# Performance work log

Hardware: AMD Instinct MI355X
Metric: run time of the kernel (lower is better)

The kernel has to match this reference:

```python
import jax, jax.numpy as jnp
import numpy as np

DIM = 192
HEADS = 8
B, H, W = 2, 256, 256
CPH = DIM // HEADS  # 24 channels per head
EPS = 1e-12

_SOB_DX = np.array([[1, 0, 1], [-2, 0, 2], [-1, 0, 1]], np.float32)
_SOB_DY = np.array([[1, -2, -1], [0, 0, 0], [1, 2, 1]], np.float32)


def _conv2d(x, w, pad, groups=1):
    return jax.lax.conv_general_dilated(
        x, w, window_strides=(1, 1), padding=[(pad, pad), (pad, pad)],
        dimension_numbers=('NCHW', 'OIHW', 'NCHW'), feature_group_count=groups)


def _l2norm(t):
    n = jnp.sqrt(jnp.sum(t * t, axis=-1, keepdims=True))
    return t / jnp.maximum(n, EPS)


def _topk_masked_softmax(attn, k):
    # attn: [B, HEADS, C, C]; keep top-k entries per row, softmax over them.
    b, h, c, _ = attn.shape
    idx = jax.lax.top_k(attn, k)[1]                      # [B,H,C,k]
    flat_idx = idx.reshape(-1, k)
    rows = jnp.arange(flat_idx.shape[0])[:, None]
    mask = jnp.zeros((b * h * c, c), bool).at[rows, flat_idx].set(True)
    masked = jnp.where(mask.reshape(attn.shape), attn, -jnp.inf)
    return jax.nn.softmax(masked, axis=-1)


def setup_inputs() -> dict:
    key = jax.random.key(0)
    ks = jax.random.split(key, 6)
    s = 0.02
    return {
        'x': jax.random.normal(ks[0], (B, DIM, H, W), jnp.float32),
        'q_w': jax.random.normal(ks[1], (DIM, DIM, 1, 1), jnp.float32) * s,
        'q_dw': jax.random.normal(ks[2], (DIM, 1, 3, 3), jnp.float32) * s,
        'kv_w': jax.random.normal(ks[3], (2 * DIM, DIM, 1, 1), jnp.float32) * s,
        'kv_dw': jax.random.normal(ks[4], (2 * DIM, 1, 3, 3), jnp.float32) * s,
        'proj_w': jax.random.normal(ks[5], (DIM, DIM, 1, 1), jnp.float32) * s,
        'temperature': jnp.ones((HEADS, 1, 1), jnp.float32),
        'a1': jnp.full((1,), 0.2, jnp.float32),
        'a2': jnp.full((1,), 0.2, jnp.float32),
        'a3': jnp.full((1,), 0.2, jnp.float32),
        'a4': jnp.full((1,), 0.2, jnp.float32),
    }


def reference(x, q_w, q_dw, kv_w, kv_dw, proj_w, temperature, a1, a2, a3, a4):
    b, c, h, w = x.shape
    # Sob: dense (dim,dim,3,3) Sobel convs (kernel broadcast over all in-channels)
    dx_w = jnp.broadcast_to(jnp.asarray(_SOB_DX), (c, c, 3, 3))
    dy_w = jnp.broadcast_to(jnp.asarray(_SOB_DY), (c, c, 3, 3))
    dx = _conv2d(x, dx_w, 1)
    dy = _conv2d(x, dy_w, 1)

    q_s = _conv2d(_conv2d(dx + dy, q_w, 0), q_dw, 1, groups=c)
    kv = _conv2d(_conv2d(x, kv_w, 0), kv_dw, 1, groups=2 * c)
    k_, v = kv[:, :c], kv[:, c:]

    hw = h * w
    q_s = _l2norm(q_s.reshape(b, HEADS, CPH, hw))
    k_ = _l2norm(k_.reshape(b, HEADS, CPH, hw))
    v = v.reshape(b, HEADS, CPH, hw)

    # channel attention: [B, HEADS, C, C]
    attn = jnp.einsum('bhcn,bhdn->bhcd', q_s, k_) * temperature

    C = CPH
    out = (a1 * (_topk_masked_softmax(attn, int(C / 2)) @ v)
           + a2 * (_topk_masked_softmax(attn, int(C * 2 / 3)) @ v)
           + a3 * (_topk_masked_softmax(attn, int(C * 3 / 4)) @ v)
           + a4 * (_topk_masked_softmax(attn, int(C * 4 / 5)) @ v))

    out = out.reshape(b, c, h, w)
    return _conv2d(out, proj_w, 0)
```

## Files before the change

### kernel.cpp

```cpp
#include <hip/hip_runtime.h>
#include <math.h>

#define NH 8
#define HWv 65536
#define C2 384

typedef __attribute__((ext_vector_type(8))) short bf16x8;
typedef __attribute__((ext_vector_type(4))) float f32x4;

__device__ __forceinline__ float bf2f(unsigned short u) {
    union { unsigned int i; float f; } v; v.i = ((unsigned int)u) << 16; return v.f;
}
__device__ __forceinline__ unsigned short f2bf(float f) {
    union { float f; unsigned int i; } v; v.f = f;
    unsigned int r = v.i + 0x7fff + ((v.i >> 16) & 1);
    return (unsigned short)(r >> 16);
}
__device__ __forceinline__ float hi_of(float a) {
    union { float f; unsigned int i; } u; u.f = a; u.i &= 0xffff0000u; return u.f;
}
__device__ __forceinline__ unsigned short hi16(float a) {
    union { float f; unsigned int i; } u; u.f = a; return (unsigned short)(u.i >> 16);
}
__device__ __forceinline__ unsigned int pack_hi2(float a, float b) {
    union { float f; unsigned int i; } ua, ub; ua.f = a; ub.f = b;
    return (ua.i >> 16) | (ub.i & 0xffff0000u);
}
__device__ __forceinline__ void gld16(const void* g, void* l) {
    __builtin_amdgcn_global_load_lds(
        (const __attribute__((address_space(1))) unsigned int*)g,
        (__attribute__((address_space(3))) unsigned int*)l, 16, 0, 0);
}
__device__ __forceinline__ int rot4(int lb, int row) {
    return (lb + row + (row >> 2)) & 3;
}

__global__ __launch_bounds__(256) void k_wprep(const float* __restrict__ w,
                                               const float* __restrict__ qw,
                                               unsigned short* __restrict__ oh,
                                               unsigned short* __restrict__ ol,
                                               float* __restrict__ qs) {
    if (blockIdx.x == 288) {
        const int o = threadIdx.x;
        if (o < 192) {
            float s = 0.f;
            for (int i = 0; i < 192; ++i) s += qw[(size_t)o * 192 + i];
            qs[o] = s;
        }
        return;
    }
    const int i = blockIdx.x * 256 + threadIdx.x;
    const int e = i & 7, jp = (i >> 3) & 3, rowidx = i >> 5;
    const int o = rowidx % 384, ks = rowidx / 384;
    const int lb = (jp - o - (o >> 2)) & 3;
    const int k = ks * 32 + (lb << 3) + e;
    const float v = w[(size_t)o * 192 + k];
    const unsigned short h = f2bf(v);
    oh[i] = h;
    ol[i] = f2bf(v - bf2f(h));
}

__global__ __launch_bounds__(256, 3) void k_gemm(const float* __restrict__ x,
                                                 const unsigned short* __restrict__ wh,
                                                 const unsigned short* __restrict__ wl,
                                                 unsigned short* __restrict__ t,
                                                 float* __restrict__ s) {
    const int l = blockIdx.x;
    const int xcd = l & 7, idx = l >> 3;
    const int pxtile = xcd * 64 + (idx >> 1);
    const int half = idx & 1;
    const int b = blockIdx.z;
    const int p0 = pxtile * 128;
    const int woff = half * 192;
    const int tid = threadIdx.x;
    const int lane = tid & 63, wv = tid >> 6;
    __shared__ __align__(16) char SU[40960];
    unsigned short* Xh  = (unsigned short*)SU;
    unsigned short* Xl  = Xh + 128 * 32;
    unsigned short* Whs = Xl + 128 * 32;
    unsigned short* Wls = Whs + 192 * 32;
    unsigned short* Ts  = (unsigned short*)SU;
    float* Ls = (float*)(SU + 26624);
    f32x4 acc[2][12];
#pragma unroll
    for (int m = 0; m < 2; ++m)
#pragma unroll
        for (int n = 0; n < 12; ++n) acc[m][n] = (f32x4){0.f, 0.f, 0.f, 0.f};
    const int px = tid & 127, cg = tid >> 7;
    const float* xb = x + (size_t)b * 192 * HWv + p0 + px;
    const int r = lane & 15, g = lane >> 4;
    const int pbx0 = rot4(2 * cg, px);
    const int pbx1 = rot4(2 * cg + 1, px);
    float csum = 0.f;
    for (int ks = 0; ks < 6; ++ks) {
        const int k0 = ks * 32;
        __syncthreads();
        {
            const char* gh  = (const char*)wh + ((size_t)(ks * 384 + woff)) * 64;
            const char* gl2 = (const char*)wl + ((size_t)(ks * 384 + woff)) * 64;
            char* lh = (char*)Whs;
            char* ll = (char*)Wls;
#pragma unroll
            for (int i = 0; i < 3; ++i) {
                const int chunk = (i * 4 + wv) * 1024;
                gld16(gh + chunk + lane * 16, lh + chunk);
                gld16(gl2 + chunk + lane * 16, ll + chunk);
            }
        }
        {
            unsigned int ph[8], pl[8];
#pragma unroll
            for (int i2 = 0; i2 < 8; ++i2) {
                const int c0 = k0 + cg * 16 + i2 * 2;
                const float v0 = xb[(size_t)c0 * HWv];
                const float v1 = xb[(size_t)(c0 + 1) * HWv];
                csum += v0 + v1;
                ph[i2] = pack_hi2(v0, v1);
                pl[i2] = pack_hi2(v0 - hi_of(v0), v1 - hi_of(v1));
            }
            *(uint4*)&Xh[px * 32 + pbx0 * 8] = make_uint4(ph[0], ph[1], ph[2], ph[3]);
            *(uint4*)&Xh[px * 32 + pbx1 * 8] = make_uint4(ph[4], ph[5], ph[6], ph[7]);
            *(uint4*)&Xl[px * 32 + pbx0 * 8] = make_uint4(pl[0], pl[1], pl[2], pl[3]);
            *(uint4*)&Xl[px * 32 + pbx1 * 8] = make_uint4(pl[4], pl[5], pl[6], pl[7]);
        }
        __syncthreads();
        bf16x8 ah[2], al[2];
#pragma unroll
        for (int m = 0; m < 2; ++m) {
            const int row = wv * 32 + m * 16 + r;
            const int ro = rot4(g, row) * 8;
            ah[m] = *(const bf16x8*)&Xh[row * 32 + ro];
            al[m] = *(const bf16x8*)&Xl[row * 32 + ro];
        }
#pragma unroll
        for (int n = 0; n < 12; ++n) {
            const int row = n * 16 + r;
            const int ro = rot4(g, row) * 8;
            const bf16x8 bh = *(const bf16x8*)&Whs[row * 32 + ro];
            const bf16x8 bl = *(const bf16x8*)&Wls[row * 32 + ro];
#pragma unroll
            for (int m = 0; m < 2; ++m) {
                acc[m][n] = __builtin_amdgcn_mfma_f32_16x16x32_bf16(ah[m], bh, acc[m][n], 0, 0, 0);
                acc[m][n] = __builtin_amdgcn_mfma_f32_16x16x32_bf16(ah[m], bl, acc[m][n], 0, 0, 0);
                acc[m][n] = __builtin_amdgcn_mfma_f32_16x16x32_bf16(al[m], bh, acc[m][n], 0, 0, 0);
            }
        }
    }
    __syncthreads();
    if (half == 0) Ls[cg * 128 + px] = csum;
    __syncthreads();
    if (half == 0 && tid < 128)
        s[((size_t)b << 16) + p0 + tid] = Ls[tid] + Ls[128 + tid];
    unsigned short* tb = t + (size_t)b * HWv * C2;
#pragma unroll
    for (int ph2 = 0; ph2 < 2; ++ph2) {
        __syncthreads();
        if ((wv >> 1) == ph2) {
            const int baser = (wv & 1) * 32;
#pragma unroll
            for (int m = 0; m < 2; ++m)
#pragma unroll
                for (int n = 0; n < 12; ++n)
#pragma unroll
                    for (int rr = 0; rr < 4; ++rr)
                        Ts[(baser + m * 16 + g * 4 + rr) * 200 + n * 16 + r] =
                            f2bf(acc[m][n][rr]);
        }
        __syncthreads();
        for (int i = tid; i < 1536; i += 256) {
            const int pxl = i / 24, cho = (i % 24) * 8;
            unsigned short* dst = tb + (size_t)(p0 + ph2 * 64 + pxl) * C2 + woff + cho;
            *(uint4*)dst = *(const uint4*)&Ts[pxl * 200 + cho];
        }
    }
}

__global__ __launch_bounds__(256) void k_attn(const unsigned short* __restrict__ t,
                                              const float* __restrict__ sbuf,
                                              const float* __restrict__ qsum,
                                              const float* __restrict__ qdw,
                                              const float* __restrict__ kvdw,
                                              float* __restrict__ part) {
    const int z = blockIdx.z, b = z >> 3, h = z & 7;
    const int tid = threadIdx.x;
    const int lane = tid & 63, wv = tid >> 6;
    __shared__ __align__(16) char U[50688];
    float* ehalo = (float*)U;
    float* Thalo = (float*)(U + 1296);
    float* shalo = (float*)(U + 32496);
    unsigned short* QKh = (unsigned short*)U;
    unsigned short* QKl = QKh + 48 * 264;
    float* Pp = (float*)U;
    __shared__ float qdwl[216], kdwl[216], qsml[24];
    for (int i = tid; i < 456; i += 256) {
        if (i < 216) qdwl[i] = qdw[h * 216 + i];
        else if (i < 432) kdwl[i - 216] = kvdw[h * 216 + (i - 216)];
        else qsml[i - 432] = qsum[h * 24 + (i - 432)];
    }
    f32x4 acc[6];
#pragma unroll
    for (int tl = 0; tl < 6; ++tl) acc[tl] = (f32x4){0.f, 0.f, 0.f, 0.f};
    const int lr = tid >> 4, lc = tid & 15;
    const int r = lane & 15, g = lane >> 4;
    for (int st = 0; st < 4; ++st) {
        const int tx0 = (blockIdx.x * 2 + (st & 1)) * 16;
        const int ty0 = (blockIdx.y * 2 + (st >> 1)) * 16;
        __syncthreads();
        for (int i = tid; i < 400; i += 256) {
            const int rr = i / 20, cc = i % 20;
            const int y = ty0 - 2 + rr, xx = tx0 - 2 + cc;
            shalo[i] = (y >= 0 && y < 256 && xx >= 0 && xx < 256)
                           ? sbuf[((size_t)b << 16) + y * 256 + xx] : 0.f;
        }
        for (int i = tid; i < 972; i += 256) {
            const int p = i / 3, seg = i % 3;
            const int rr = p / 18, cc = p % 18;
            const int y = ty0 - 1 + rr, xx = tx0 - 1 + cc;
            if (y >= 0 && y < 256 && xx >= 0 && xx < 256) {
                const unsigned short* src =
                    t + ((size_t)b * HWv + y * 256 + xx) * C2 + h * 24 + seg * 8;
                const uint4 v = *(const uint4*)src;
                Thalo[(seg * 8 + 0) * 325 + p] = bf2f((unsigned short)(v.x & 0xffff));
                Thalo[(seg * 8 + 1) * 325 + p] = bf2f((unsigned short)(v.x >> 16));
                Thalo[(seg * 8 + 2) * 325 + p] = bf2f((unsigned short)(v.y & 0xffff));
                Thalo[(seg * 8 + 3) * 325 + p] = bf2f((unsigned short)(v.y >> 16));
                Thalo[(seg * 8 + 4) * 325 + p] = bf2f((unsigned short)(v.z & 0xffff));
                Thalo[(seg * 8 + 5) * 325 + p] = bf2f((unsigned short)(v.z >> 16));
                Thalo[(seg * 8 + 6) * 325 + p] = bf2f((unsigned short)(v.w & 0xffff));
                Thalo[(seg * 8 + 7) * 325 + p] = bf2f((unsigned short)(v.w >> 16));
            } else {
#pragma unroll
                for (int j = 0; j < 8; ++j) Thalo[(seg * 8 + j) * 325 + p] = 0.f;
            }
        }
        __syncthreads();
        for (int i = tid; i < 324; i += 256) {
            const int rr = i / 18, cc = i % 18;
            const int y = ty0 - 1 + rr, xx = tx0 - 1 + cc;
            const float v = (((((shalo[rr * 20 + cc]
                              - shalo[rr * 20 + cc + 1])
                              - shalo[(rr + 1) * 20 + cc])
                              + shalo[(rr + 1) * 20 + cc + 2])
                              + shalo[(rr + 2) * 20 + cc + 1])
                              + shalo[(rr + 2) * 20 + cc + 2]);
            ehalo[i] = (y >= 0 && y < 256 && xx >= 0 && xx < 256) ? 2.f * v : 0.f;
        }
        __syncthreads();
        float qreg[24], kreg[24];
#pragma unroll
        for (int c = 0; c < 24; ++c) {
            float aq = 0.f, ak = 0.f;
#pragma unroll
            for (int dy = 0; dy < 3; ++dy)
#pragma unroll
                for (int dx = 0; dx < 3; ++dx) {
                    aq = fmaf(qdwl[c * 9 + dy * 3 + dx], ehalo[(lr + dy) * 18 + lc + dx], aq);
                    ak = fmaf(kdwl[c * 9 + dy * 3 + dx], Thalo[c * 325 + (lr + dy) * 18 + lc + dx], ak);
                }
            qreg[c] = qsml[c] * aq;
            kreg[c] = ak;
        }
        __syncthreads();
#pragma unroll
        for (int c = 0; c < 24; ++c) {
            const float q = qreg[c], kv = kreg[c];
            QKh[c * 264 + tid] = hi16(q);
            QKl[c * 264 + tid] = hi16(q - hi_of(q));
            QKh[(24 + c) * 264 + tid] = hi16(kv);
            QKl[(24 + c) * 264 + tid] = hi16(kv - hi_of(kv));
        }
        __syncthreads();
#pragma unroll
        for (int c2 = 0; c2 < 2; ++c2) {
            const int colb = (wv * 2 + c2) * 32 + g * 8;
            bf16x8 fh[3], fl[3];
#pragma unroll
            for (int rt = 0; rt < 3; ++rt) {
                fh[rt] = *(const bf16x8*)&QKh[(rt * 16 + r) * 264 + colb];
                fl[rt] = *(const bf16x8*)&QKl[(rt * 16 + r) * 264 + colb];
            }
#define GRAM(T, A, B) \
    acc[T] = __builtin_amdgcn_mfma_f32_16x16x32_bf16(fh[A], fh[B], acc[T], 0, 0, 0); \
    acc[T] = __builtin_amdgcn_mfma_f32_16x16x32_bf16(fh[A], fl[B], acc[T], 0, 0, 0); \
    acc[T] = __builtin_amdgcn_mfma_f32_16x16x32_bf16(fl[A], fh[B], acc[T], 0, 0, 0);
            GRAM(0, 0, 0) GRAM(1, 0, 1) GRAM(2, 0, 2)
            GRAM(3, 1, 1) GRAM(4, 1, 2) GRAM(5, 2, 2)
#undef GRAM
        }
    }
    __syncthreads();
#pragma unroll
    for (int tl = 0; tl < 6; ++tl)
#pragma unroll
        for (int reg = 0; reg < 4; ++reg)
            Pp[wv * 1536 + tl * 256 + (g * 4 + reg) * 16 + r] = acc[tl][reg];
    __syncthreads();
    float* dst = part + ((size_t)z * 64 + blockIdx.y * 8 + blockIdx.x) * 1536;
    for (int i = tid; i < 1536; i += 256)
        dst[i] = Pp[i] + Pp[1536 + i] + Pp[3072 + i] + Pp[4608 + i];
}

__device__ __forceinline__ int gidx(int i, int j) {
    const int rt = i >> 4, ct = j >> 4;
    const int tl = (rt == 0) ? ct : (rt == 1 ? 2 + ct : 5);
    return tl * 256 + (i & 15) * 16 + (j & 15);
}

__global__ __launch_bounds__(256) void k_redcomb(const float* __restrict__ part,
                                                 const float* __restrict__ temp,
                                                 const float* __restrict__ a1,
                                                 const float* __restrict__ a2,
                                                 const float* __restrict__ a3,
                                                 const float* __restrict__ a4,
                                                 float* __restrict__ Wg) {
    const int z = blockIdx.x, b = z >> 3, h = z & 7;
    const int tid = threadIdx.x;
    __shared__ float S[1536];
    __shared__ float att[24][24];
    __shared__ float nq[24], nk[24];
    for (int i = tid; i < 1536; i += 256) {
        float sum = 0.f;
        const float* p = part + (size_t)z * 64 * 1536 + i;
        for (int blk = 0; blk < 64; ++blk) sum += p[(size_t)blk * 1536];
        S[i] = sum;
    }
    __syncthreads();
    if (tid < 24) nq[tid] = fmaxf(sqrtf(S[gidx(tid, tid)]), 1e-12f);
    else if (tid >= 32 && tid < 56) {
        const int d = tid - 32;
        nk[d] = fmaxf(sqrtf(S[gidx(24 + d, 24 + d)]), 1e-12f);
    }
    __syncthreads();
    const float tp = temp[h];
    for (int op = tid; op < 576; op += 256) {
        const int c = op / 24, d = op % 24;
        att[c][d] = S[gidx(c, 24 + d)] * tp / (nq[c] * nk[d]);
    }
    __syncthreads();
    if (tid < 24) {
        const int c = tid;
        float v[24];
#pragma unroll
        for (int d = 0; d < 24; ++d) v[d] = att[c][d];
        int rank[24];
#pragma unroll
        for (int d = 0; d < 24; ++d) {
            int rr = 0;
#pragma unroll
            for (int d2 = 0; d2 < 24; ++d2)
                rr += (v[d2] > v[d]) || (v[d2] == v[d] && d2 < d);
            rank[d] = rr;
        }
        const int ks[4] = {12, 16, 18, 19};
        const float as[4] = {a1[0], a2[0], a3[0], a4[0]};
        float w[24] = {};
        for (int ti = 0; ti < 4; ++ti) {
            const int kk = ks[ti];
            float m = -1e30f;
            for (int d = 0; d < 24; ++d) if (rank[d] < kk) m = fmaxf(m, v[d]);
            float Z = 0.f, ex[24];
            for (int d = 0; d < 24; ++d) {
                ex[d] = (rank[d] < kk) ? expf(v[d] - m) : 0.f;
                Z += ex[d];
            }
            const float sc = as[ti] / Z;
            for (int d = 0; d < 24; ++d) w[d] += ex[d] * sc;
        }
        for (int d = 0; d < 24; ++d)
            Wg[(((size_t)b * NH + h) * 24 + c) * 24 + d] = w[d];
    }
}

__global__ void k_makeM(const float* __restrict__ projw, const float* __restrict__ Wg,
                        unsigned short* __restrict__ Mh, unsigned short* __restrict__ Ml) {
    const int b = blockIdx.x / 192, o = blockIdx.x % 192;
    const int j = threadIdx.x;
    const int h = j / 24, d = j % 24;
    float s = 0.f;
#pragma unroll
    for (int cc = 0; cc < 24; ++cc)
        s = fmaf(projw[(size_t)o * 192 + h * 24 + cc],
                 Wg[(((size_t)b * NH + h) * 24 + cc) * 24 + d], s);
    const unsigned short hh = f2bf(s);
    const int jg = j >> 5, jb = (j >> 3) & 3, e = j & 7;
    const int jp = rot4(jb, o);
    const size_t dst = (((size_t)b * 6 + jg) * 192 + o) * 32 + jp * 8 + e;
    Mh[dst] = hh;
    Ml[dst] = f2bf(s - bf2f(hh));
}

__global__ __launch_bounds__(256) void k_final(const unsigned short* __restrict__ t,
                                               const float* __restrict__ kvdw,
                                               const unsigned short* __restrict__ Mh,
                                               const unsigned short* __restrict__ Ml,
                                               float* __restrict__ out) {
    const int b = blockIdx.y;
    const int tile = blockIdx.x;
    const int x0 = (tile & 15) * 16, y0 = (tile >> 4) * 4;
    const int tid = threadIdx.x;
    const int lane = tid & 63, wv = tid >> 6;
    __shared__ __align__(16) unsigned short Th[108][40];
    __shared__ __align__(16) unsigned short Msh[192 * 32], Msl[192 * 32];
    __shared__ __align__(16) unsigned short Vsh[64][40], Vsl[64][40];
    __shared__ float Wdl[288];
    f32x4 acc[3][4];
#pragma unroll
    for (int m = 0; m < 3; ++m)
#pragma unroll
        for (int n = 0; n < 4; ++n) acc[m][n] = (f32x4){0.f, 0.f, 0.f, 0.f};
    const int px = tid & 63, jq = tid >> 6;
    const int lx = px & 15, ly = px >> 4;
    const int r = lane & 15, g = lane >> 4;
    for (int jg = 0; jg < 6; ++jg) {
        const int j0 = jg * 32;
        __syncthreads();
        {
            const char* gh  = (const char*)Mh + (((size_t)b * 6 + jg) * 192) * 64;
            const char* gl2 = (const char*)Ml + (((size_t)b * 6 + jg) * 192) * 64;
            char* lh = (char*)Msh;
            char* ll = (char*)Msl;
#pragma unroll
            for (int i = 0; i < 3; ++i) {
                const int chunk = (i * 4 + wv) * 1024;
                gld16(gh + chunk + lane * 16, lh + chunk);
                gld16(gl2 + chunk + lane * 16, ll + chunk);
            }
        }
        if (tid < 216) {
            const int hp = tid >> 1, half = tid & 1;
            const int hy = hp / 18, hx = hp % 18;
            const int y = y0 - 1 + hy, xx = x0 - 1 + hx;
            uint4 v0 = make_uint4(0, 0, 0, 0), v1 = make_uint4(0, 0, 0, 0);
            if (y >= 0 && y < 256 && xx >= 0 && xx < 256) {
                const unsigned short* src =
                    t + ((size_t)b * HWv + y * 256 + xx) * C2 + 192 + j0 + half * 16;
                v0 = *(const uint4*)src;
                v1 = *(const uint4*)(src + 8);
            }
            *(uint4*)&Th[hp][half * 16] = v0;
            *(uint4*)&Th[hp][half * 16 + 8] = v1;
        }
        for (int i = tid; i < 288; i += 256) Wdl[i] = kvdw[1728 + jg * 288 + i];
        __syncthreads();
        {
            float vv[8] = {0.f, 0.f, 0.f, 0.f, 0.f, 0.f, 0.f, 0.f};
#pragma unroll
            for (int dy = 0; dy < 3; ++dy)
#pragma unroll
                for (int dx = 0; dx < 3; ++dx) {
                    const int hp = (ly + dy) * 18 + lx + dx;
                    const uint4 tv = *(const uint4*)&Th[hp][jq * 8];
                    float tf[8];
                    tf[0] = bf2f((unsigned short)(tv.x & 0xffff));
                    tf[1] = bf2f((unsigned short)(tv.x >> 16));
                    tf[2] = bf2f((unsigned short)(tv.y & 0xffff));
                    tf[3] = bf2f((unsigned short)(tv.y >> 16));
                    tf[4] = bf2f((unsigned short)(tv.z & 0xffff));
                    tf[5] = bf2f((unsigned short)(tv.z >> 16));
                    tf[6] = bf2f((unsigned short)(tv.w & 0xffff));
                    tf[7] = bf2f((unsigned short)(tv.w >> 16));
                    const int tap = dy * 3 + dx;
#pragma unroll
                    for (int jj = 0; jj < 8; ++jj)
                        vv[jj] = fmaf(Wdl[(jq * 8 + jj) * 9 + tap], tf[jj], vv[jj]);
                }
            unsigned int ph[4], pl[4];
#pragma unroll
            for (int i2 = 0; i2 < 4; ++i2) {
                const float a = vv[i2 * 2], c = vv[i2 * 2 + 1];
                ph[i2] = pack_hi2(a, c);
                pl[i2] = pack_hi2(a - hi_of(a), c - hi_of(c));
            }
            *(uint4*)&Vsh[px][jq * 8] = make_uint4(ph[0], ph[1], ph[2], ph[3]);
            *(uint4*)&Vsl[px][jq * 8] = make_uint4(pl[0], pl[1], pl[2], pl[3]);
        }
        __syncthreads();
        bf16x8 bh[4], bl[4];
#pragma unroll
        for (int n = 0; n < 4; ++n) {
            bh[n] = *(const bf16x8*)&Vsh[n * 16 + r][g * 8];
            bl[n] = *(const bf16x8*)&Vsl[n * 16 + r][g * 8];
        }
#pragma unroll
        for (int m = 0; m < 3; ++m) {
            const int row = wv * 48 + m * 16 + r;
            const int ro = rot4(g, row) * 8;
            const bf16x8 ah = *(const bf16x8*)&Msh[row * 32 + ro];
            const bf16x8 al = *(const bf16x8*)&Msl[row * 32 + ro];
#pragma unroll
            for (int n = 0; n < 4; ++n) {
                acc[m][n] = __builtin_amdgcn_mfma_f32_16x16x32_bf16(ah, bh[n], acc[m][n], 0, 0, 0);
                acc[m][n] = __builtin_amdgcn_mfma_f32_16x16x32_bf16(ah, bl[n], acc[m][n], 0, 0, 0);
                acc[m][n] = __builtin_amdgcn_mfma_f32_16x16x32_bf16(al, bh[n], acc[m][n], 0, 0, 0);
            }
        }
    }
#pragma unroll
    for (int m = 0; m < 3; ++m) {
        const int o = wv * 48 + m * 16 + g * 4;
#pragma unroll
        for (int n = 0; n < 4; ++n) {
            const int p = (y0 + n) * 256 + x0 + r;
#pragma unroll
            for (int rr = 0; rr < 4; ++rr)
                out[((size_t)b * 192 + o + rr) * HWv + p] = acc[m][n][rr];
        }
    }
}


extern "C" void kernel_launch(void* const* d_in, const int* in_sizes, int n_in,
                              void* d_out, int out_size, void* d_ws, size_t ws_size,
                              hipStream_t stream) {
    (void)in_sizes; (void)n_in; (void)out_size;
    const float* x     = (const float*)d_in[0];
    const float* qw    = (const float*)d_in[1];
    const float* qdw   = (const float*)d_in[2];
    const float* kvw   = (const float*)d_in[3];
    const float* kvdw  = (const float*)d_in[4];
    const float* projw = (const float*)d_in[5];
    const float* temp  = (const float*)d_in[6];
    const float* a1    = (const float*)d_in[7];
    const float* a2    = (const float*)d_in[8];
    const float* a3    = (const float*)d_in[9];
    const float* a4    = (const float*)d_in[10];
    float* out = (float*)d_out;

    const size_t T_EL = (size_t)2 * HWv * C2;
    const size_t needB = T_EL * 2
                       + (size_t)(131072 + 131072 + 192 + 1572864 + 24576 + 9216) * 4
                       + (size_t)(73728 * 4) * 2;
    if (ws_size < needB) return;
    unsigned short* t = (unsigned short*)d_ws;
    float* s    = (float*)(t + T_EL);
    float* e    = s + 131072;
    float* qsum = e + 131072;
    float* part = qsum + 192;
    float* accS = part + 1572864;
    float* Wg   = accS + 24576;
    unsigned short* wh = (unsigned short*)(Wg + 9216);
    unsigned short* wl = wh + 73728;
    unsigned short* Mh = wl + 73728;
    unsigned short* Ml = Mh + 73728;

    k_wprep<<<289, 256, 0, stream>>>(kvw, qw, wh, wl, qsum);
    k_gemm<<<dim3(1024, 1, 2), 256, 0, stream>>>(x, wh, wl, t, s);
    k_attn<<<dim3(8, 8, 16), 256, 0, stream>>>(t, s, qsum, qdw, kvdw, part);
    k_redcomb<<<16, 256, 0, stream>>>(part, temp, a1, a2, a3, a4, Wg);
    k_makeM<<<384, 192, 0, stream>>>(projw, Wg, Mh, Ml);
    k_final<<<dim3(1024, 2), 256, 0, stream>>>(t, kvdw, Mh, Ml, out);
}
```

Baseline: 256.0 us.

## Double-buffer GEMM K-loop to overlap global loads with MFMA compute

The k_gemm main loop now uses two LDS buffers. It prefetches the next K-slice of x into registers and issues async weight loads into the alternate buffer, then runs the MFMAs on the current one, and packs x into the next buffer afterwards. This drops one barrier per iteration and hides global-load latency behind compute. In exchange, LDS per block doubles to 80 KB and launch bounds drop from 3 to 2 blocks per SM, which lowers occupancy and raises register pressure from the extra 16 prefetch registers.

```diff
diff --git a/kernel.cpp b/kernel.cpp
--- a/kernel.cpp
+++ b/kernel.cpp
@@ -60,7 +60,7 @@
     ol[i] = f2bf(v - bf2f(h));
 }
 
-__global__ __launch_bounds__(256, 3) void k_gemm(const float* __restrict__ x,
+__global__ __launch_bounds__(256, 2) void k_gemm(const float* __restrict__ x,
                                                  const unsigned short* __restrict__ wh,
                                                  const unsigned short* __restrict__ wl,
                                                  unsigned short* __restrict__ t,
@@ -74,12 +74,8 @@
     const int woff = half * 192;
     const int tid = threadIdx.x;
     const int lane = tid & 63, wv = tid >> 6;
-    __shared__ __align__(16) char SU[40960];
-    unsigned short* Xh  = (unsigned short*)SU;
-    unsigned short* Xl  = Xh + 128 * 32;
-    unsigned short* Whs = Xl + 128 * 32;
-    unsigned short* Wls = Whs + 192 * 32;
-    unsigned short* Ts  = (unsigned short*)SU;
+    __shared__ __align__(16) char SU[81920];
+    unsigned short* Ts = (unsigned short*)SU;
     float* Ls = (float*)(SU + 26624);
     f32x4 acc[2][12];
 #pragma unroll
@@ -92,38 +88,62 @@
     const int pbx0 = rot4(2 * cg, px);
     const int pbx1 = rot4(2 * cg + 1, px);
     float csum = 0.f;
+    float xr[16];
+
+    auto load_x = [&](int ks) {
+#pragma unroll
+        for (int i2 = 0; i2 < 8; ++i2) {
+            const int c0 = ks * 32 + cg * 16 + i2 * 2;
+            xr[2 * i2]     = xb[(size_t)c0 * HWv];
+            xr[2 * i2 + 1] = xb[(size_t)(c0 + 1) * HWv];
+        }
+    };
+    auto stage_w = [&](int ks, char* base) {
+        const char* gh  = (const char*)wh + ((size_t)(ks * 384 + woff)) * 64;
+        const char* gl2 = (const char*)wl + ((size_t)(ks * 384 + woff)) * 64;
+        char* lh = base + 16384;
+        char* ll = base + 28672;
+#pragma unroll
+        for (int i = 0; i < 3; ++i) {
+            const int chunk = (i * 4 + wv) * 1024;
+            gld16(gh + chunk + lane * 16, lh + chunk);
+            gld16(gl2 + chunk + lane * 16, ll + chunk);
+        }
+    };
+    auto pack_x = [&](char* base) {
+        unsigned short* Xh = (unsigned short*)base;
+        unsigned short* Xl = (unsigned short*)(base + 8192);
+        unsigned int ph[8], pl[8];
+#pragma unroll
+        for (int i2 = 0; i2 < 8; ++i2) {
+            const float v0 = xr[2 * i2], v1 = xr[2 * i2 + 1];
+            csum += v0 + v1;
+            ph[i2] = pack_hi2(v0, v1);
+            pl[i2] = pack_hi2(v0 - hi_of(v0), v1 - hi_of(v1));
+        }
+        *(uint4*)&Xh[px * 32 + pbx0 * 8] = make_uint4(ph[0], ph[1], ph[2], ph[3]);
+        *(uint4*)&Xh[px * 32 + pbx1 * 8] = make_uint4(ph[4], ph[5], ph[6], ph[7]);
+        *(uint4*)&Xl[px * 32 + pbx0 * 8] = make_uint4(pl[0], pl[1], pl[2], pl[3]);
+        *(uint4*)&Xl[px * 32 + pbx1 * 8] = make_uint4(pl[4], pl[5], pl[6], pl[7]);
+    };
+
+    load_x(0);
+    stage_w(0, SU);
+    pack_x(SU);
+    __syncthreads();
+
+#pragma unroll
     for (int ks = 0; ks < 6; ++ks) {
-        const int k0 = ks * 32;
-        __syncthreads();
-        {
-            const char* gh  = (const char*)wh + ((size_t)(ks * 384 + woff)) * 64;
-            const char* gl2 = (const char*)wl + ((size_t)(ks * 384 + woff)) * 64;
-            char* lh = (char*)Whs;
-            char* ll = (char*)Wls;
-#pragma unroll
-            for (int i = 0; i < 3; ++i) {
-                const int chunk = (i * 4 + wv) * 1024;
-                gld16(gh + chunk + lane * 16, lh + chunk);
-                gld16(gl2 + chunk + lane * 16, ll + chunk);
-            }
-        }
-        {
-            unsigned int ph[8], pl[8];
-#pragma unroll
-            for (int i2 = 0; i2 < 8; ++i2) {
-                const int c0 = k0 + cg * 16 + i2 * 2;
-                const float v0 = xb[(size_t)c0 * HWv];
-                const float v1 = xb[(size_t)(c0 + 1) * HWv];
-                csum += v0 + v1;
-                ph[i2] = pack_hi2(v0, v1);
-                pl[i2] = pack_hi2(v0 - hi_of(v0), v1 - hi_of(v1));
-            }
-            *(uint4*)&Xh[px * 32 + pbx0 * 8] = make_uint4(ph[0], ph[1], ph[2], ph[3]);
-            *(uint4*)&Xh[px * 32 + pbx1 * 8] = make_uint4(ph[4], ph[5], ph[6], ph[7]);
-            *(uint4*)&Xl[px * 32 + pbx0 * 8] = make_uint4(pl[0], pl[1], pl[2], pl[3]);
-            *(uint4*)&Xl[px * 32 + pbx1 * 8] = make_uint4(pl[4], pl[5], pl[6], pl[7]);
-        }
-        __syncthreads();
+        char* bc = SU + (ks & 1) * 40960;
+        char* bn = SU + ((ks & 1) ^ 1) * 40960;
+        if (ks < 5) {
+            load_x(ks + 1);
+            stage_w(ks + 1, bn);
+        }
+        unsigned short* Xh  = (unsigned short*)bc;
+        unsigned short* Xl  = (unsigned short*)(bc + 8192);
+        unsigned short* Whs = (unsigned short*)(bc + 16384);
+        unsigned short* Wls = (unsigned short*)(bc + 28672);
         bf16x8 ah[2], al[2];
 #pragma unroll
         for (int m = 0; m < 2; ++m) {
@@ -145,8 +165,10 @@
                 acc[m][n] = __builtin_amdgcn_mfma_f32_16x16x32_bf16(al[m], bh, acc[m][n], 0, 0, 0);
             }
         }
-    }
-    __syncthreads();
+        if (ks < 5) pack_x(bn);
+        __syncthreads();
+    }
+
     if (half == 0) Ls[cg * 128 + px] = csum;
     __syncthreads();
     if (half == 0 && tid < 128)
```

Result: slower. 263.7 us (+3.0%).

## Split k_gemm tile across 8 waves in a 4x2 wave grid

Applied to the files above, without the earlier changes.

Doubles the k_gemm block from 256 to 512 threads. Each wave now computes a 32x96 output sub-tile instead of 32x192, which halves the accumulator registers per wave and raises the wave count available for latency hiding. The global-to-LDS staging of the X slices and weight chunks is redistributed over the eight waves, and the per-pixel channel sums are reduced across four channel groups. The trade-off is that each wave reloads its A fragments for fewer MFMAs, and block-wide barriers now span more waves.

```diff
diff --git a/kernel.cpp b/kernel.cpp
--- a/kernel.cpp
+++ b/kernel.cpp
@@ -60,7 +60,7 @@
     ol[i] = f2bf(v - bf2f(h));
 }
 
-__global__ __launch_bounds__(256, 3) void k_gemm(const float* __restrict__ x,
+__global__ __launch_bounds__(512, 4) void k_gemm(const float* __restrict__ x,
                                                  const unsigned short* __restrict__ wh,
                                                  const unsigned short* __restrict__ wl,
                                                  unsigned short* __restrict__ t,
@@ -74,6 +74,7 @@
     const int woff = half * 192;
     const int tid = threadIdx.x;
     const int lane = tid & 63, wv = tid >> 6;
+    const int wm = wv & 3, wn = wv >> 2;
     __shared__ __align__(16) char SU[40960];
     unsigned short* Xh  = (unsigned short*)SU;
     unsigned short* Xl  = Xh + 128 * 32;
@@ -81,16 +82,15 @@
     unsigned short* Wls = Whs + 192 * 32;
     unsigned short* Ts  = (unsigned short*)SU;
     float* Ls = (float*)(SU + 26624);
-    f32x4 acc[2][12];
+    f32x4 acc[2][6];
 #pragma unroll
     for (int m = 0; m < 2; ++m)
 #pragma unroll
-        for (int n = 0; n < 12; ++n) acc[m][n] = (f32x4){0.f, 0.f, 0.f, 0.f};
+        for (int n = 0; n < 6; ++n) acc[m][n] = (f32x4){0.f, 0.f, 0.f, 0.f};
     const int px = tid & 127, cg = tid >> 7;
     const float* xb = x + (size_t)b * 192 * HWv + p0 + px;
     const int r = lane & 15, g = lane >> 4;
-    const int pbx0 = rot4(2 * cg, px);
-    const int pbx1 = rot4(2 * cg + 1, px);
+    const int pbx = rot4(cg, px);
     float csum = 0.f;
     for (int ks = 0; ks < 6; ++ks) {
         const int k0 = ks * 32;
@@ -98,43 +98,39 @@
         {
             const char* gh  = (const char*)wh + ((size_t)(ks * 384 + woff)) * 64;
             const char* gl2 = (const char*)wl + ((size_t)(ks * 384 + woff)) * 64;
-            char* lh = (char*)Whs;
-            char* ll = (char*)Wls;
 #pragma unroll
             for (int i = 0; i < 3; ++i) {
-                const int chunk = (i * 4 + wv) * 1024;
-                gld16(gh + chunk + lane * 16, lh + chunk);
-                gld16(gl2 + chunk + lane * 16, ll + chunk);
+                const int ch = i * 8 + wv;
+                if (ch < 12) gld16(gh + ch * 1024 + lane * 16, (char*)Whs + ch * 1024);
+                else gld16(gl2 + (ch - 12) * 1024 + lane * 16, (char*)Wls + (ch - 12) * 1024);
             }
         }
         {
-            unsigned int ph[8], pl[8];
-#pragma unroll
-            for (int i2 = 0; i2 < 8; ++i2) {
-                const int c0 = k0 + cg * 16 + i2 * 2;
+            unsigned int ph[4], pl[4];
+#pragma unroll
+            for (int i2 = 0; i2 < 4; ++i2) {
+                const int c0 = k0 + cg * 8 + i2 * 2;
                 const float v0 = xb[(size_t)c0 * HWv];
                 const float v1 = xb[(size_t)(c0 + 1) * HWv];
                 csum += v0 + v1;
                 ph[i2] = pack_hi2(v0, v1);
                 pl[i2] = pack_hi2(v0 - hi_of(v0), v1 - hi_of(v1));
             }
-            *(uint4*)&Xh[px * 32 + pbx0 * 8] = make_uint4(ph[0], ph[1], ph[2], ph[3]);
-            *(uint4*)&Xh[px * 32 + pbx1 * 8] = make_uint4(ph[4], ph[5], ph[6], ph[7]);
-            *(uint4*)&Xl[px * 32 + pbx0 * 8] = make_uint4(pl[0], pl[1], pl[2], pl[3]);
-            *(uint4*)&Xl[px * 32 + pbx1 * 8] = make_uint4(pl[4], pl[5], pl[6], pl[7]);
+            *(uint4*)&Xh[px * 32 + pbx * 8] = make_uint4(ph[0], ph[1], ph[2], ph[3]);
+            *(uint4*)&Xl[px * 32 + pbx * 8] = make_uint4(pl[0], pl[1], pl[2], pl[3]);
         }
         __syncthreads();
         bf16x8 ah[2], al[2];
 #pragma unroll
         for (int m = 0; m < 2; ++m) {
-            const int row = wv * 32 + m * 16 + r;
+            const int row = wm * 32 + m * 16 + r;
             const int ro = rot4(g, row) * 8;
             ah[m] = *(const bf16x8*)&Xh[row * 32 + ro];
             al[m] = *(const bf16x8*)&Xl[row * 32 + ro];
         }
 #pragma unroll
-        for (int n = 0; n < 12; ++n) {
-            const int row = n * 16 + r;
+        for (int n = 0; n < 6; ++n) {
+            const int row = wn * 96 + n * 16 + r;
             const int ro = rot4(g, row) * 8;
             const bf16x8 bh = *(const bf16x8*)&Whs[row * 32 + ro];
             const bf16x8 bl = *(const bf16x8*)&Wls[row * 32 + ro];
@@ -147,27 +143,27 @@
         }
     }
     __syncthreads();
-    if (half == 0) Ls[cg * 128 + px] = csum;
+    Ls[cg * 128 + px] = csum;
     __syncthreads();
     if (half == 0 && tid < 128)
-        s[((size_t)b << 16) + p0 + tid] = Ls[tid] + Ls[128 + tid];
+        s[((size_t)b << 16) + p0 + tid] = Ls[tid] + Ls[128 + tid] + Ls[256 + tid] + Ls[384 + tid];
     unsigned short* tb = t + (size_t)b * HWv * C2;
 #pragma unroll
     for (int ph2 = 0; ph2 < 2; ++ph2) {
         __syncthreads();
-        if ((wv >> 1) == ph2) {
-            const int baser = (wv & 1) * 32;
+        if ((wm >> 1) == ph2) {
+            const int baser = (wm & 1) * 32;
 #pragma unroll
             for (int m = 0; m < 2; ++m)
 #pragma unroll
-                for (int n = 0; n < 12; ++n)
+                for (int n = 0; n < 6; ++n)
 #pragma unroll
                     for (int rr = 0; rr < 4; ++rr)
-                        Ts[(baser + m * 16 + g * 4 + rr) * 200 + n * 16 + r] =
+                        Ts[(baser + m * 16 + g * 4 + rr) * 200 + wn * 96 + n * 16 + r] =
                             f2bf(acc[m][n][rr]);
         }
         __syncthreads();
-        for (int i = tid; i < 1536; i += 256) {
+        for (int i = tid; i < 1536; i += 512) {
             const int pxl = i / 24, cho = (i % 24) * 8;
             unsigned short* dst = tb + (size_t)(p0 + ph2 * 64 + pxl) * C2 + woff + cho;
             *(uint4*)dst = *(const uint4*)&Ts[pxl * 200 + cho];
@@ -544,7 +540,7 @@
     unsigned short* Ml = Mh + 73728;
 
     k_wprep<<<289, 256, 0, stream>>>(kvw, qw, wh, wl, qsum);
-    k_gemm<<<dim3(1024, 1, 2), 256, 0, stream>>>(x, wh, wl, t, s);
+    k_gemm<<<dim3(1024, 1, 2), 512, 0, stream>>>(x, wh, wl, t, s);
     k_attn<<<dim3(8, 8, 16), 256, 0, stream>>>(t, s, qsum, qdw, kvdw, part);
     k_redcomb<<<16, 256, 0, stream>>>(part, temp, a1, a2, a3, a4, Wg);
     k_makeM<<<384, 192, 0, stream>>>(projw, Wg, Mh, Ml);
```

Result: slower. 286.5 us (+11.9%).
